# Optimization experiments

Hardware: AMD Instinct MI355X
Metric: run time of the kernel (lower is better)

The kernel has to match this reference:

```python
import jax, jax.numpy as jnp
import numpy as np

B, DIM, HEADS, H, W = 8, 384, 8, 128, 128
EPS = 1e-12  # torch F.normalize eps


def _conv1x1(x, w):
    # x: [b,c,h,w], w: [out,in] -> [b,out,h,w]
    return jnp.einsum('oc,bchw->bohw', w, x)


def _dwconv3x3(x, w):
    # depthwise 3x3, groups=DIM; w: [DIM,1,3,3]
    return jax.lax.conv_general_dilated(
        x, w, window_strides=(1, 1), padding='SAME',
        feature_group_count=DIM,
        dimension_numbers=('NCHW', 'OIHW', 'NCHW'))


def _l2norm(t):
    # F.normalize along last dim
    n = jnp.sqrt(jnp.sum(t * t, axis=-1, keepdims=True))
    return t / jnp.maximum(n, EPS)


def setup_inputs() -> dict:
    key = jax.random.key(0)
    ks = jax.random.split(key, 9)
    s = 0.02
    return {
        'x': jax.random.normal(ks[0], (B, DIM, H, W), jnp.float32),
        'w0': jax.random.normal(ks[1], (DIM, DIM), jnp.float32) * s,
        'w1': jax.random.normal(ks[2], (DIM, DIM), jnp.float32) * s,
        'w2': jax.random.normal(ks[3], (DIM, DIM), jnp.float32) * s,
        'dw0': jax.random.normal(ks[4], (DIM, 1, 3, 3), jnp.float32) * s,
        'dw1': jax.random.normal(ks[5], (DIM, 1, 3, 3), jnp.float32) * s,
        'dw2': jax.random.normal(ks[6], (DIM, 1, 3, 3), jnp.float32) * s,
        'wproj': jax.random.normal(ks[7], (DIM, DIM), jnp.float32) * s,
        'temp': jnp.ones((HEADS, 1, 1), jnp.float32),
    }


def reference(x, w0, w1, w2, dw0, dw1, dw2, wproj, temp):
    b, c, h, w = x.shape
    ch = c // HEADS
    q = _dwconv3x3(_conv1x1(x, w0), dw0)
    k = _dwconv3x3(_conv1x1(x, w1), dw1)
    v = _dwconv3x3(_conv1x1(x, w2), dw2)
    # b (head c) h w -> b head c (h w)
    q = _l2norm(q.reshape(b, HEADS, ch, h * w))
    k = _l2norm(k.reshape(b, HEADS, ch, h * w))
    v = v.reshape(b, HEADS, ch, h * w)
    attn = jax.nn.softmax(jnp.einsum('bhcn,bhdn->bhcd', q, k) * temp, axis=-1)
    out = jnp.einsum('bhcd,bhdn->bhcn', attn, v).reshape(b, c, h, w)
    return _conv1x1(out, wproj)
```

## Files before the change

kernel.cpp:

```cpp
#include <hip/hip_runtime.h>
#include <math.h>

#define DIMC 384
#define NHEADS 8
#define CHD 48
#define HWN 16384
#define IMW 128
#define PERT ((size_t)DIMC * HWN)
#define WELEM (DIMC * DIMC)
#define NB 8

typedef short short8 __attribute__((ext_vector_type(8)));
typedef unsigned short u16x8 __attribute__((ext_vector_type(8)));
typedef float f32x4 __attribute__((ext_vector_type(4)));

__device__ __forceinline__ unsigned short f2bf(float f) {
  unsigned int u = __float_as_uint(f);
  unsigned int r = (u + 0x7fffu + ((u >> 16) & 1u)) >> 16;
  return (unsigned short)r;
}
__device__ __forceinline__ float bf2f(unsigned short b) {
  return __uint_as_float(((unsigned int)b) << 16);
}
__device__ __forceinline__ void async16(const void* g, void* l) {
  __builtin_amdgcn_global_load_lds(
      (const __attribute__((address_space(1))) void*)g,
      (__attribute__((address_space(3))) void*)l, 16, 0, 0);
}

template <int OUTBF>
__device__ __forceinline__ void mfma_gemm(
    const unsigned short* __restrict__ A,
    const unsigned short* __restrict__ BT,
    void* __restrict__ Y, int obase, int nbase)
{
  __shared__ unsigned short As[3][8192];
  __shared__ unsigned short Bs[3][16384];
  const int tid = threadIdx.x;
  const int lane = tid & 63;
  const int wv = tid >> 6;
  const int wm = (wv >> 2) * 64;
  const int wn = (wv & 3) * 64;

  f32x4 acc[4][4];
#pragma unroll
  for (int i = 0; i < 4; ++i)
#pragma unroll
    for (int j = 0; j < 4; ++j) acc[i][j] = (f32x4){0.f, 0.f, 0.f, 0.f};

  const int srow = tid >> 3;
  const int sks = (tid & 7) * 8;
  const unsigned short* asrc = A + (size_t)(obase + srow) * DIMC + sks;
  const unsigned short* bsrc = BT + (size_t)(nbase + srow) * DIMC + sks;

  const int ar = wm + (lane & 15);
  const int br = wn + (lane & 15);
  const int kg = (lane >> 4) << 4;
  const int sw = (lane & 7) << 4;

#define WAITVM(n) asm volatile("s_waitcnt vmcnt(" #n ")" ::: "memory")
#define SBAR()                                 \
  do {                                         \
    __builtin_amdgcn_sched_barrier(0);         \
    __builtin_amdgcn_s_barrier();              \
    __builtin_amdgcn_sched_barrier(0);         \
  } while (0)

#define STAGE(buf, k0)                                                   \
  do {                                                                   \
    _Pragma("unroll") for (int i = 0; i < 2; ++i)                        \
        async16(asrc + (size_t)(i * 64) * DIMC + (k0),                   \
                &As[buf][(size_t)(tid + i * 512) * 8]);                  \
    _Pragma("unroll") for (int i = 0; i < 4; ++i)                        \
        async16(bsrc + (size_t)(i * 64) * DIMC + (k0),                   \
                &Bs[buf][(size_t)(tid + i * 512) * 8]);                  \
  } while (0)

#define COMPUTE(buf)                                                     \
  do {                                                                   \
    short8 af[2][4], bf[2][4];                                           \
    _Pragma("unroll") for (int kq = 0; kq < 2; ++kq) {                   \
      const int kb = kq * 64 + kg;                                       \
      _Pragma("unroll") for (int mi = 0; mi < 4; ++mi)                   \
          af[kq][mi] = *reinterpret_cast<const short8*>(                 \
              (const char*)&As[buf][0] + (ar + mi * 16) * 128 + (kb ^ sw)); \
      _Pragma("unroll") for (int ni = 0; ni < 4; ++ni)                   \
          bf[kq][ni] = *reinterpret_cast<const short8*>(                 \
              (const char*)&Bs[buf][0] + (br + ni * 16) * 128 + (kb ^ sw)); \
    }                                                                    \
    __builtin_amdgcn_s_setprio(1);                                       \
    _Pragma("unroll") for (int kq = 0; kq < 2; ++kq)                     \
      _Pragma("unroll") for (int mi = 0; mi < 4; ++mi)                   \
        _Pragma("unroll") for (int ni = 0; ni < 4; ++ni)                 \
          acc[mi][ni] = __builtin_amdgcn_mfma_f32_16x16x32_bf16(         \
              af[kq][mi], bf[kq][ni], acc[mi][ni], 0, 0, 0);             \
    __builtin_amdgcn_s_setprio(0);                                       \
  } while (0)

  STAGE(0, 0);
  STAGE(1, 64);

  WAITVM(6); SBAR(); STAGE(2, 128); COMPUTE(0);
  WAITVM(6); SBAR(); STAGE(0, 192); COMPUTE(1);
  WAITVM(6); SBAR(); STAGE(1, 256); COMPUTE(2);
  WAITVM(6); SBAR(); STAGE(2, 320); COMPUTE(0);
  WAITVM(6); SBAR(); COMPUTE(1);
  WAITVM(0); SBAR(); COMPUTE(2);

#undef STAGE
#undef COMPUTE
#undef WAITVM
#undef SBAR

  const int orow = obase + wm + ((lane >> 4) << 2);
  const int ocol = nbase + wn + (lane & 15);
#pragma unroll
  for (int mi = 0; mi < 4; ++mi)
#pragma unroll
    for (int ni = 0; ni < 4; ++ni)
#pragma unroll
      for (int r = 0; r < 4; ++r) {
        size_t off = (size_t)(orow + mi * 16 + r) * HWN + ocol + ni * 16;
        if (OUTBF) ((unsigned short*)Y)[off] = f2bf(acc[mi][ni][r]);
        else       ((float*)Y)[off] = acc[mi][ni][r];
      }
}

__global__ __launch_bounds__(512) void k_conv_mfma(
    const unsigned short* __restrict__ Wc, const unsigned short* __restrict__ XT,
    unsigned short* __restrict__ Y)
{
  int lin = ((int)blockIdx.z * 64 + blockIdx.y) * 9 + blockIdx.x;
  int swz = (lin & 7) * 576 + (lin >> 3);
  int g = swz / 9, r = swz - g * 9;
  int bb = g >> 6, nt = g & 63;
  int j = r / 3, mt = r - j * 3;
  mfma_gemm<1>(Wc + j * WELEM, XT + (size_t)bb * PERT,
               Y + (size_t)bb * 3 * PERT + (size_t)j * PERT, mt * 128, nt * 256);
}

__global__ __launch_bounds__(512) void k_final_mfma(
    const unsigned short* __restrict__ M, const unsigned short* __restrict__ vT,
    float* __restrict__ out)
{
  int lin = ((int)blockIdx.z * 64 + blockIdx.y) * 3 + blockIdx.x;
  int swz = (lin & 7) * 192 + (lin >> 3);
  int g = swz / 3, mt = swz - g * 3;
  int bb = g >> 6, nt = g & 63;
  mfma_gemm<0>(M + (size_t)bb * WELEM, vT + (size_t)bb * PERT,
               out + (size_t)bb * PERT, mt * 128, nt * 256);
}

__global__ __launch_bounds__(256) void k_transpose_x(
    const float* __restrict__ x, unsigned short* __restrict__ XT)
{
  __shared__ unsigned short S[64][72];
  int n0 = blockIdx.x * 64, c0 = blockIdx.y * 64;
  const float* xb = x + (size_t)blockIdx.z * PERT;
  unsigned short* XTb = XT + (size_t)blockIdx.z * PERT;
  int t = threadIdx.x;
  int cl = t >> 2, ns = (t & 3) * 16;
  const float* src = &xb[(size_t)(c0 + cl) * HWN + n0 + ns];
#pragma unroll
  for (int i = 0; i < 16; i += 4) {
    float4 v = *reinterpret_cast<const float4*>(&src[i]);
    S[cl][ns + i + 0] = f2bf(v.x);
    S[cl][ns + i + 1] = f2bf(v.y);
    S[cl][ns + i + 2] = f2bf(v.z);
    S[cl][ns + i + 3] = f2bf(v.w);
  }
  __syncthreads();
  int nl = t >> 2, cs = (t & 3) * 16;
  unsigned short tmp[16];
#pragma unroll
  for (int i = 0; i < 16; ++i) tmp[i] = S[cs + i][nl];
  u16x8 p0, p1;
#pragma unroll
  for (int i = 0; i < 8; ++i) { p0[i] = tmp[i]; p1[i] = tmp[8 + i]; }
  char* rowb = (char*)XTb + (size_t)(n0 + nl) * (DIMC * 2);
  int cb = (c0 + cs) * 2;
  int sw = (nl & 7) << 4;
  *reinterpret_cast<u16x8*>(rowb + ((cb) ^ sw)) = p0;
  *reinterpret_cast<u16x8*>(rowb + ((cb + 16) ^ sw)) = p1;
}

__global__ __launch_bounds__(256) void k_transpose_v(
    const unsigned short* __restrict__ qkv, unsigned short* __restrict__ vT)
{
  __shared__ unsigned short S[64][72];
  int n0 = blockIdx.x * 64, c0 = blockIdx.y * 64;
  const unsigned short* v = qkv + (size_t)blockIdx.z * 3 * PERT + 2 * PERT;
  unsigned short* vTb = vT + (size_t)blockIdx.z * PERT;
  int t = threadIdx.x;
  int cl = t >> 2, ns = (t & 3) * 16;
  const unsigned short* src = &v[(size_t)(c0 + cl) * HWN + n0 + ns];
  *reinterpret_cast<u16x8*>(&S[cl][ns]) = *reinterpret_cast<const u16x8*>(&src[0]);
  *reinterpret_cast<u16x8*>(&S[cl][ns + 8]) = *reinterpret_cast<const u16x8*>(&src[8]);
  __syncthreads();
  int nl = t >> 2, cs = (t & 3) * 16;
  unsigned short tmp[16];
#pragma unroll
  for (int i = 0; i < 16; ++i) tmp[i] = S[cs + i][nl];
  u16x8 p0, p1;
#pragma unroll
  for (int i = 0; i < 8; ++i) { p0[i] = tmp[i]; p1[i] = tmp[8 + i]; }
  char* rowb = (char*)vTb + (size_t)(n0 + nl) * (DIMC * 2);
  int cb = (c0 + cs) * 2;
  int sw = (nl & 7) << 4;
  *reinterpret_cast<u16x8*>(rowb + ((cb) ^ sw)) = p0;
  *reinterpret_cast<u16x8*>(rowb + ((cb + 16) ^ sw)) = p1;
}

__global__ __launch_bounds__(256) void k_convert_w(
    const float* __restrict__ w0, const float* __restrict__ w1,
    const float* __restrict__ w2, unsigned short* __restrict__ Wc)
{
  int idx = blockIdx.x * 256 + threadIdx.x;
  int j = idx / WELEM, r = idx - j * WELEM;
  int m = r / DIMC, k = r - m * DIMC;
  const float* s = (j == 0) ? w0 : (j == 1) ? w1 : w2;
  int kd = (k & ~63) | ((k & 63) ^ ((m & 7) << 3));
  Wc[j * WELEM + m * DIMC + kd] = f2bf(s[r]);
}

__global__ __launch_bounds__(256) void k_dwconv(
    const unsigned short* __restrict__ Yin, const float* __restrict__ dw0,
    const float* __restrict__ dw1, const float* __restrict__ dw2,
    unsigned short* __restrict__ Zout, float* __restrict__ partial)
{
  __shared__ float red[4];
  int gid = blockIdx.x * 256 + threadIdx.x;
  int plane = gid >> 10;
  int rem = gid & 1023;
  int pl = plane % (3 * DIMC);
  int j = pl / DIMC;
  int c = pl - j * DIMC;
  int h = rem >> 3;
  int wg = (rem & 7) << 4;
  int lane = threadIdx.x & 63;
  const float* dw = ((j == 0) ? dw0 : (j == 1) ? dw1 : dw2) + c * 9;
  const unsigned short* src = Yin + (size_t)plane * HWN;

  float acc[16];
#pragma unroll
  for (int i = 0; i < 16; ++i) acc[i] = 0.f;

#pragma unroll
  for (int dy = -1; dy <= 1; ++dy) {
    int hh = h + dy;
    bool valid = (hh >= 0) && (hh < IMW);
    float mf[16];
    if (valid) {
      const unsigned short* row = src + hh * IMW + wg;
      u16x8 a0 = *reinterpret_cast<const u16x8*>(row);
      u16x8 a1 = *reinterpret_cast<const u16x8*>(row + 8);
#pragma unroll
      for (int i = 0; i < 8; ++i) { mf[i] = bf2f(a0[i]); mf[8 + i] = bf2f(a1[i]); }
    } else {
#pragma unroll
      for (int i = 0; i < 16; ++i) mf[i] = 0.f;
    }
    float lf = __shfl_up(mf[15], 1);
    float rf = __shfl_down(mf[0], 1);
    if ((lane & 7) == 0) lf = 0.f;
    if ((lane & 7) == 7) rf = 0.f;
    float t0 = dw[(dy + 1) * 3], t1 = dw[(dy + 1) * 3 + 1], t2 = dw[(dy + 1) * 3 + 2];
    acc[0] = fmaf(lf, t0, fmaf(mf[0], t1, fmaf(mf[1], t2, acc[0])));
#pragma unroll
    for (int i = 1; i < 15; ++i)
      acc[i] = fmaf(mf[i - 1], t0, fmaf(mf[i], t1, fmaf(mf[i + 1], t2, acc[i])));
    acc[15] = fmaf(mf[14], t0, fmaf(mf[15], t1, fmaf(rf, t2, acc[15])));
  }

  u16x8 o0, o1;
#pragma unroll
  for (int i = 0; i < 8; ++i) { o0[i] = f2bf(acc[i]); o1[i] = f2bf(acc[8 + i]); }
  unsigned short* dst = Zout + (size_t)plane * HWN + h * IMW + wg;
  *reinterpret_cast<u16x8*>(dst) = o0;
  *reinterpret_cast<u16x8*>(dst + 8) = o1;

  if (j < 2) {
    float s = 0.f;
#pragma unroll
    for (int i = 0; i < 16; ++i) s = fmaf(acc[i], acc[i], s);
#pragma unroll
    for (int off = 32; off > 0; off >>= 1) s += __shfl_down(s, off);
    if ((threadIdx.x & 63) == 0) red[threadIdx.x >> 6] = s;
    __syncthreads();
    if (threadIdx.x == 0)
      partial[blockIdx.x] = red[0] + red[1] + red[2] + red[3];
  }
}

__global__ __launch_bounds__(256) void k_qk_mfma(
    const unsigned short* __restrict__ qkv, float* __restrict__ Spart)
{
  __shared__ float Sred[4][2304];
  int blk = blockIdx.x;
  int b = blk >> 6, h = (blk >> 3) & 7, slice = blk & 7;
  int tid = threadIdx.x, lane = tid & 63, w = tid >> 6;
  const unsigned short* qb = qkv + ((size_t)b * 3 * DIMC + h * CHD) * HWN;
  const unsigned short* kb = qb + (size_t)DIMC * HWN;
  const int row = lane & 15;
  const int ko = (lane >> 4) << 3;
  const int n0 = slice * 2048 + w * 512;

  f32x4 acc[3][3];
#pragma unroll
  for (int i = 0; i < 3; ++i)
#pragma unroll
    for (int j = 0; j < 3; ++j) acc[i][j] = (f32x4){0.f, 0.f, 0.f, 0.f};

  for (int ns = n0; ns < n0 + 512; ns += 32) {
    short8 aq[3], bk[3];
#pragma unroll
    for (int mi = 0; mi < 3; ++mi)
      aq[mi] = *reinterpret_cast<const short8*>(&qb[(size_t)(mi * 16 + row) * HWN + ns + ko]);
#pragma unroll
    for (int ni = 0; ni < 3; ++ni)
      bk[ni] = *reinterpret_cast<const short8*>(&kb[(size_t)(ni * 16 + row) * HWN + ns + ko]);
#pragma unroll
    for (int mi = 0; mi < 3; ++mi)
#pragma unroll
      for (int ni = 0; ni < 3; ++ni)
        acc[mi][ni] = __builtin_amdgcn_mfma_f32_16x16x32_bf16(
            aq[mi], bk[ni], acc[mi][ni], 0, 0, 0);
  }
  const int c0 = (lane >> 4) << 2;
#pragma unroll
  for (int mi = 0; mi < 3; ++mi)
#pragma unroll
    for (int ni = 0; ni < 3; ++ni)
#pragma unroll
      for (int r = 0; r < 4; ++r)
        Sred[w][(mi * 16 + c0 + r) * 48 + ni * 16 + row] = acc[mi][ni][r];
  __syncthreads();
  float* dst = Spart + (size_t)blk * 2304;
#pragma unroll
  for (int i = 0; i < 9; ++i) {
    int e = tid + i * 256;
    dst[e] = Sred[0][e] + Sred[1][e] + Sred[2][e] + Sred[3][e];
  }
}

__global__ __launch_bounds__(384) void k_attn_sm(
    const float* __restrict__ Spart, const float* __restrict__ partial,
    const float* __restrict__ temp, float* __restrict__ Aat)
{
  __shared__ float sk[DIMC];
  int b = blockIdx.x, t = threadIdx.x;
  int h = t / CHD, c = t - h * CHD;
  float sq = 0.f, skk = 0.f;
#pragma unroll
  for (int s = 0; s < 4; ++s) {
    sq  += partial[((size_t)b * 1152 + t) * 4 + s];
    skk += partial[((size_t)b * 1152 + DIMC + t) * 4 + s];
  }
  sk[t] = 1.f / fmaxf(sqrtf(skk), 1e-12f);
  float invq = 1.f / fmaxf(sqrtf(sq), 1e-12f);
  __syncthreads();
  float vals[CHD];
#pragma unroll
  for (int d = 0; d < CHD; ++d) vals[d] = 0.f;
  for (int sl = 0; sl < 8; ++sl) {
    const float* sp = Spart + (size_t)(b * 64 + h * 8 + sl) * 2304 + c * 48;
#pragma unroll
    for (int d = 0; d < CHD; ++d) vals[d] += sp[d];
  }
  float tp = temp[h];
  float vq = invq * tp;
  float mx = -1e30f;
#pragma unroll
  for (int d = 0; d < CHD; ++d) {
    vals[d] *= vq * sk[h * CHD + d];
    mx = fmaxf(mx, vals[d]);
  }
  float sum = 0.f;
#pragma unroll
  for (int d = 0; d < CHD; ++d) { vals[d] = expf(vals[d] - mx); sum += vals[d]; }
  float inv = 1.f / sum;
  float* Arow = Aat + ((size_t)(b * 8 + h) * 48 + c) * 48;
#pragma unroll
  for (int d = 0; d < CHD; ++d) Arow[d] = vals[d] * inv;
}

__global__ __launch_bounds__(256) void k_combine(
    const float* __restrict__ wproj, const float* __restrict__ Aat,
    unsigned short* __restrict__ M)
{
  int idx = blockIdx.x * 256 + threadIdx.x;
  int b = idx / WELEM;
  int r2 = idx - b * WELEM;
  int o = r2 / DIMC;
  int dg = r2 - o * DIMC;
  int h = dg / CHD, d = dg - h * CHD;
  const float* wrow = wproj + (size_t)o * DIMC + h * CHD;
  const float* Acol = Aat + (size_t)b * DIMC * CHD + (size_t)(h * CHD) * CHD + d;
  float s = 0.f;
#pragma unroll
  for (int c = 0; c < CHD; ++c)
    s = fmaf(wrow[c], Acol[c * CHD], s);
  int dd = (dg & ~63) | ((dg & 63) ^ ((o & 7) << 3));
  M[b * WELEM + o * DIMC + dd] = f2bf(s);
}

extern "C" void kernel_launch(void* const* d_in, const int* in_sizes, int n_in,
                              void* d_out, int out_size, void* d_ws, size_t ws_size,
                              hipStream_t stream)
{
  const float* x     = (const float*)d_in[0];
  const float* w0    = (const float*)d_in[1];
  const float* w1    = (const float*)d_in[2];
  const float* w2    = (const float*)d_in[3];
  const float* dw0   = (const float*)d_in[4];
  const float* dw1   = (const float*)d_in[5];
  const float* dw2   = (const float*)d_in[6];
  const float* wproj = (const float*)d_in[7];
  const float* temp  = (const float*)d_in[8];
  float* out = (float*)d_out;

  char* p = (char*)d_ws;
  unsigned short* Wc     = (unsigned short*)p;  p += (size_t)3 * WELEM * 2;
  unsigned short* XT     = (unsigned short*)p;  p += (size_t)NB * PERT * 2;
  unsigned short* q0k0v0 = (unsigned short*)p;  p += (size_t)NB * 3 * PERT * 2;
  unsigned short* qkv    = (unsigned short*)p;  p += (size_t)NB * 3 * PERT * 2;
  float* Spart   = (float*)p;  p += (size_t)512 * 2304 * 4;
  float* Aat     = (float*)p;  p += (size_t)NB * DIMC * CHD * 4;
  float* partial = (float*)p;  p += (size_t)NB * 3 * DIMC * 4 * 4;
  unsigned short* Mbf = (unsigned short*)p;
  unsigned short* vT = XT;

  k_convert_w<<<(3 * WELEM + 255) / 256, 256, 0, stream>>>(w0, w1, w2, Wc);
  k_transpose_x<<<dim3(256, 6, NB), 256, 0, stream>>>(x, XT);
  k_conv_mfma<<<dim3(9, 64, NB), 512, 0, stream>>>(Wc, XT, q0k0v0);
  k_dwconv<<<NB * 3 * DIMC * 4, 256, 0, stream>>>(q0k0v0, dw0, dw1, dw2, qkv, partial);
  k_transpose_v<<<dim3(256, 6, NB), 256, 0, stream>>>(qkv, vT);
  k_qk_mfma<<<512, 256, 0, stream>>>(qkv, Spart);
  k_attn_sm<<<NB, 384, 0, stream>>>(Spart, partial, temp, Aat);
  k_combine<<<(NB * WELEM) / 256, 256, 0, stream>>>(wproj, Aat, Mbf);
  k_final_mfma<<<dim3(3, 64, NB), 512, 0, stream>>>(Mbf, vT, out);
  (void)in_sizes; (void)n_in; (void)out_size; (void)ws_size;
}
```

Baseline: 650.6 us.

## Shrink GEMM tiles to 128x128 with double buffering and LDS-staged coalesced epilogue

Both MFMA GEMM kernels drop from 512-thread 128x256 tiles with triple-buffered LDS to 256-thread 128x128 tiles with double buffering in a 64KB LDS region, doubling the grid. The epilogue now stages accumulators through padded LDS and writes whole rows with 16-byte vector stores, replacing scattered per-element global stores. The smaller tile and fewer LDS bytes per block are meant to raise occupancy and coalesce output writes. In exchange the pipeline waits for vmcnt(0) every step, so loads overlap compute less, and each B element is reloaded more often.

Result: slower. 724.8 us (+11.4%).

```diff
diff --git a/kernel.cpp b/kernel.cpp
--- a/kernel.cpp
+++ b/kernel.cpp
@@ -34,13 +34,12 @@
     const unsigned short* __restrict__ BT,
     void* __restrict__ Y, int obase, int nbase)
 {
-  __shared__ unsigned short As[3][8192];
-  __shared__ unsigned short Bs[3][16384];
+  __shared__ unsigned char LDSRAW[65536];
   const int tid = threadIdx.x;
   const int lane = tid & 63;
   const int wv = tid >> 6;
-  const int wm = (wv >> 2) * 64;
-  const int wn = (wv & 3) * 64;
+  const int wm = (wv >> 1) * 64;
+  const int wn = (wv & 1) * 64;
 
   f32x4 acc[4][4];
 #pragma unroll
@@ -66,89 +65,122 @@
     __builtin_amdgcn_sched_barrier(0);         \
   } while (0)
 
-#define STAGE(buf, k0)                                                   \
-  do {                                                                   \
-    _Pragma("unroll") for (int i = 0; i < 2; ++i)                        \
-        async16(asrc + (size_t)(i * 64) * DIMC + (k0),                   \
-                &As[buf][(size_t)(tid + i * 512) * 8]);                  \
-    _Pragma("unroll") for (int i = 0; i < 4; ++i)                        \
-        async16(bsrc + (size_t)(i * 64) * DIMC + (k0),                   \
-                &Bs[buf][(size_t)(tid + i * 512) * 8]);                  \
+#define STAGE(buf, k0)                                                    \
+  do {                                                                    \
+    unsigned short* Adst = (unsigned short*)LDSRAW + (buf) * 8192;        \
+    unsigned short* Bdst = (unsigned short*)(LDSRAW + 32768) + (buf) * 8192; \
+    _Pragma("unroll") for (int i = 0; i < 4; ++i)                         \
+        async16(asrc + (size_t)(i * 32) * DIMC + (k0),                    \
+                Adst + (size_t)(tid + i * 256) * 8);                      \
+    _Pragma("unroll") for (int i = 0; i < 4; ++i)                         \
+        async16(bsrc + (size_t)(i * 32) * DIMC + (k0),                    \
+                Bdst + (size_t)(tid + i * 256) * 8);                      \
   } while (0)
 
-#define COMPUTE(buf)                                                     \
-  do {                                                                   \
-    short8 af[2][4], bf[2][4];                                           \
-    _Pragma("unroll") for (int kq = 0; kq < 2; ++kq) {                   \
-      const int kb = kq * 64 + kg;                                       \
-      _Pragma("unroll") for (int mi = 0; mi < 4; ++mi)                   \
-          af[kq][mi] = *reinterpret_cast<const short8*>(                 \
-              (const char*)&As[buf][0] + (ar + mi * 16) * 128 + (kb ^ sw)); \
-      _Pragma("unroll") for (int ni = 0; ni < 4; ++ni)                   \
-          bf[kq][ni] = *reinterpret_cast<const short8*>(                 \
-              (const char*)&Bs[buf][0] + (br + ni * 16) * 128 + (kb ^ sw)); \
-    }                                                                    \
-    __builtin_amdgcn_s_setprio(1);                                       \
-    _Pragma("unroll") for (int kq = 0; kq < 2; ++kq)                     \
-      _Pragma("unroll") for (int mi = 0; mi < 4; ++mi)                   \
-        _Pragma("unroll") for (int ni = 0; ni < 4; ++ni)                 \
-          acc[mi][ni] = __builtin_amdgcn_mfma_f32_16x16x32_bf16(         \
-              af[kq][mi], bf[kq][ni], acc[mi][ni], 0, 0, 0);             \
-    __builtin_amdgcn_s_setprio(0);                                       \
+#define COMPUTE(buf)                                                      \
+  do {                                                                    \
+    const char* Ab = (const char*)LDSRAW + (buf) * 16384;                 \
+    const char* Bb = (const char*)LDSRAW + 32768 + (buf) * 16384;         \
+    short8 af[2][4], bf[2][4];                                            \
+    _Pragma("unroll") for (int kq = 0; kq < 2; ++kq) {                    \
+      const int kb = kq * 64 + kg;                                        \
+      _Pragma("unroll") for (int mi = 0; mi < 4; ++mi)                    \
+          af[kq][mi] = *reinterpret_cast<const short8*>(                  \
+              Ab + (ar + mi * 16) * 128 + (kb ^ sw));                     \
+      _Pragma("unroll") for (int ni = 0; ni < 4; ++ni)                    \
+          bf[kq][ni] = *reinterpret_cast<const short8*>(                  \
+              Bb + (br + ni * 16) * 128 + (kb ^ sw));                     \
+    }                                                                     \
+    __builtin_amdgcn_s_setprio(1);                                        \
+    _Pragma("unroll") for (int kq = 0; kq < 2; ++kq)                      \
+      _Pragma("unroll") for (int mi = 0; mi < 4; ++mi)                    \
+        _Pragma("unroll") for (int ni = 0; ni < 4; ++ni)                  \
+          acc[mi][ni] = __builtin_amdgcn_mfma_f32_16x16x32_bf16(          \
+              af[kq][mi], bf[kq][ni], acc[mi][ni], 0, 0, 0);              \
+    __builtin_amdgcn_s_setprio(0);                                        \
   } while (0)
 
   STAGE(0, 0);
-  STAGE(1, 64);
-
-  WAITVM(6); SBAR(); STAGE(2, 128); COMPUTE(0);
-  WAITVM(6); SBAR(); STAGE(0, 192); COMPUTE(1);
-  WAITVM(6); SBAR(); STAGE(1, 256); COMPUTE(2);
-  WAITVM(6); SBAR(); STAGE(2, 320); COMPUTE(0);
-  WAITVM(6); SBAR(); COMPUTE(1);
-  WAITVM(0); SBAR(); COMPUTE(2);
+  WAITVM(0); SBAR(); STAGE(1, 64);  COMPUTE(0);
+  WAITVM(0); SBAR(); STAGE(0, 128); COMPUTE(1);
+  WAITVM(0); SBAR(); STAGE(1, 192); COMPUTE(0);
+  WAITVM(0); SBAR(); STAGE(0, 256); COMPUTE(1);
+  WAITVM(0); SBAR(); STAGE(1, 320); COMPUTE(0);
+  WAITVM(0); SBAR();                COMPUTE(1);
+  __syncthreads();
 
 #undef STAGE
 #undef COMPUTE
+
+  const int crow = wm + ((lane >> 4) << 2);
+  const int ccol = wn + (lane & 15);
+
+  if (OUTBF) {
+    unsigned short* C16 = (unsigned short*)LDSRAW;
+#pragma unroll
+    for (int mi = 0; mi < 4; ++mi)
+#pragma unroll
+      for (int ni = 0; ni < 4; ++ni)
+#pragma unroll
+        for (int r = 0; r < 4; ++r)
+          C16[(crow + mi * 16 + r) * 134 + ccol + ni * 16] = f2bf(acc[mi][ni][r]);
+    __syncthreads();
+    const int row = tid >> 1, col = (tid & 1) << 6;
+    const unsigned short* srcl = C16 + row * 134 + col;
+    unsigned short* dst = (unsigned short*)Y + (size_t)(obase + row) * HWN + nbase + col;
+#pragma unroll
+    for (int i = 0; i < 8; ++i)
+      *reinterpret_cast<u16x8*>(dst + i * 8) = *reinterpret_cast<const u16x8*>(srcl + i * 8);
+  } else {
+    float* C32 = (float*)LDSRAW;
+#pragma unroll
+    for (int p = 0; p < 2; ++p) {
+      if (wn == p * 64) {
+#pragma unroll
+        for (int mi = 0; mi < 4; ++mi)
+#pragma unroll
+          for (int ni = 0; ni < 4; ++ni)
+#pragma unroll
+            for (int r = 0; r < 4; ++r)
+              C32[(crow + mi * 16 + r) * 66 + (lane & 15) + ni * 16] = acc[mi][ni][r];
+      }
+      __syncthreads();
+      const int row = tid >> 1, colseg = (tid & 1) << 5;
+      const float* srcl = C32 + row * 66 + colseg;
+      float* dst = (float*)Y + (size_t)(obase + row) * HWN + nbase + p * 64 + colseg;
+#pragma unroll
+      for (int i = 0; i < 8; ++i)
+        *reinterpret_cast<f32x4*>(dst + i * 4) = *reinterpret_cast<const f32x4*>(srcl + i * 4);
+      __syncthreads();
+    }
+  }
 #undef WAITVM
 #undef SBAR
-
-  const int orow = obase + wm + ((lane >> 4) << 2);
-  const int ocol = nbase + wn + (lane & 15);
-#pragma unroll
-  for (int mi = 0; mi < 4; ++mi)
-#pragma unroll
-    for (int ni = 0; ni < 4; ++ni)
-#pragma unroll
-      for (int r = 0; r < 4; ++r) {
-        size_t off = (size_t)(orow + mi * 16 + r) * HWN + ocol + ni * 16;
-        if (OUTBF) ((unsigned short*)Y)[off] = f2bf(acc[mi][ni][r]);
-        else       ((float*)Y)[off] = acc[mi][ni][r];
-      }
-}
-
-__global__ __launch_bounds__(512) void k_conv_mfma(
+}
+
+__global__ __launch_bounds__(256) void k_conv_mfma(
     const unsigned short* __restrict__ Wc, const unsigned short* __restrict__ XT,
     unsigned short* __restrict__ Y)
 {
-  int lin = ((int)blockIdx.z * 64 + blockIdx.y) * 9 + blockIdx.x;
-  int swz = (lin & 7) * 576 + (lin >> 3);
+  int lin = ((int)blockIdx.z * 128 + blockIdx.y) * 9 + blockIdx.x;
+  int swz = (lin & 7) * 1152 + (lin >> 3);
   int g = swz / 9, r = swz - g * 9;
-  int bb = g >> 6, nt = g & 63;
+  int bb = g >> 7, nt = g & 127;
   int j = r / 3, mt = r - j * 3;
   mfma_gemm<1>(Wc + j * WELEM, XT + (size_t)bb * PERT,
-               Y + (size_t)bb * 3 * PERT + (size_t)j * PERT, mt * 128, nt * 256);
-}
-
-__global__ __launch_bounds__(512) void k_final_mfma(
+               Y + (size_t)bb * 3 * PERT + (size_t)j * PERT, mt * 128, nt * 128);
+}
+
+__global__ __launch_bounds__(256) void k_final_mfma(
     const unsigned short* __restrict__ M, const unsigned short* __restrict__ vT,
     float* __restrict__ out)
 {
-  int lin = ((int)blockIdx.z * 64 + blockIdx.y) * 3 + blockIdx.x;
-  int swz = (lin & 7) * 192 + (lin >> 3);
+  int lin = ((int)blockIdx.z * 128 + blockIdx.y) * 3 + blockIdx.x;
+  int swz = (lin & 7) * 384 + (lin >> 3);
   int g = swz / 3, mt = swz - g * 3;
-  int bb = g >> 6, nt = g & 63;
+  int bb = g >> 7, nt = g & 127;
   mfma_gemm<0>(M + (size_t)bb * WELEM, vT + (size_t)bb * PERT,
-               out + (size_t)bb * PERT, mt * 128, nt * 256);
+               out + (size_t)bb * PERT, mt * 128, nt * 128);
 }
 
 __global__ __launch_bounds__(256) void k_transpose_x(
@@ -432,12 +464,12 @@
 
   k_convert_w<<<(3 * WELEM + 255) / 256, 256, 0, stream>>>(w0, w1, w2, Wc);
   k_transpose_x<<<dim3(256, 6, NB), 256, 0, stream>>>(x, XT);
-  k_conv_mfma<<<dim3(9, 64, NB), 512, 0, stream>>>(Wc, XT, q0k0v0);
+  k_conv_mfma<<<dim3(9, 128, NB), 256, 0, stream>>>(Wc, XT, q0k0v0);
   k_dwconv<<<NB * 3 * DIMC * 4, 256, 0, stream>>>(q0k0v0, dw0, dw1, dw2, qkv, partial);
   k_transpose_v<<<dim3(256, 6, NB), 256, 0, stream>>>(qkv, vT);
   k_qk_mfma<<<512, 256, 0, stream>>>(qkv, Spart);
   k_attn_sm<<<NB, 384, 0, stream>>>(Spart, partial, temp, Aat);
   k_combine<<<(NB * WELEM) / 256, 256, 0, stream>>>(wproj, Aat, Mbf);
-  k_final_mfma<<<dim3(3, 64, NB), 512, 0, stream>>>(Mbf, vT, out);
+  k_final_mfma<<<dim3(3, 128, NB), 256, 0, stream>>>(Mbf, vT, out);
   (void)in_sizes; (void)n_in; (void)out_size; (void)ws_size;
 }
```

## Load GEMM A-operand weights directly into registers, bypassing LDS staging

Applied to the files above, without the earlier changes.

The MFMA GEMM no longer stages the weight (A) tiles through LDS. Each wave loads its A fragments straight from global memory into two double-buffered register sets, interleaved with the existing triple-buffered LDS pipeline for B. The pre-swizzle of weights in k_convert_w and k_combine is removed because the A path no longer reads from swizzled LDS, and the vmcnt waits are retuned for the extra loads. This cuts LDS traffic and footprint for A, relying on the small weight matrices being served from cache. In exchange it raises register pressure and issues more, less coalesced global loads per wave.

New measurement: 760.8 us. 1.17x slower.

```diff
diff --git a/kernel.cpp b/kernel.cpp
--- a/kernel.cpp
+++ b/kernel.cpp
@@ -34,7 +34,6 @@
     const unsigned short* __restrict__ BT,
     void* __restrict__ Y, int obase, int nbase)
 {
-  __shared__ unsigned short As[3][8192];
   __shared__ unsigned short Bs[3][16384];
   const int tid = threadIdx.x;
   const int lane = tid & 63;
@@ -50,13 +49,16 @@
 
   const int srow = tid >> 3;
   const int sks = (tid & 7) * 8;
-  const unsigned short* asrc = A + (size_t)(obase + srow) * DIMC + sks;
   const unsigned short* bsrc = BT + (size_t)(nbase + srow) * DIMC + sks;
 
-  const int ar = wm + (lane & 15);
+  const unsigned short* aP =
+      A + (size_t)(obase + wm + (lane & 15)) * DIMC + ((lane >> 4) << 3);
+
   const int br = wn + (lane & 15);
   const int kg = (lane >> 4) << 4;
   const int sw = (lane & 7) << 4;
+
+  short8 sA0[2][4], sA1[2][4];
 
 #define WAITVM(n) asm volatile("s_waitcnt vmcnt(" #n ")" ::: "memory")
 #define SBAR()                                 \
@@ -66,24 +68,26 @@
     __builtin_amdgcn_sched_barrier(0);         \
   } while (0)
 
-#define STAGE(buf, k0)                                                   \
+#define STAGE_B(buf, k0)                                                 \
   do {                                                                   \
-    _Pragma("unroll") for (int i = 0; i < 2; ++i)                        \
-        async16(asrc + (size_t)(i * 64) * DIMC + (k0),                   \
-                &As[buf][(size_t)(tid + i * 512) * 8]);                  \
     _Pragma("unroll") for (int i = 0; i < 4; ++i)                        \
         async16(bsrc + (size_t)(i * 64) * DIMC + (k0),                   \
                 &Bs[buf][(size_t)(tid + i * 512) * 8]);                  \
   } while (0)
 
-#define COMPUTE(buf)                                                     \
+#define LOADA(set, k0)                                                   \
   do {                                                                   \
-    short8 af[2][4], bf[2][4];                                           \
+    _Pragma("unroll") for (int kq = 0; kq < 2; ++kq)                     \
+      _Pragma("unroll") for (int mi = 0; mi < 4; ++mi)                   \
+        set[kq][mi] = *reinterpret_cast<const short8*>(                  \
+            aP + (size_t)(mi * 16) * DIMC + (k0) + kq * 32);             \
+  } while (0)
+
+#define COMPUTE(buf, set)                                                \
+  do {                                                                   \
+    short8 bf[2][4];                                                     \
     _Pragma("unroll") for (int kq = 0; kq < 2; ++kq) {                   \
       const int kb = kq * 64 + kg;                                       \
-      _Pragma("unroll") for (int mi = 0; mi < 4; ++mi)                   \
-          af[kq][mi] = *reinterpret_cast<const short8*>(                 \
-              (const char*)&As[buf][0] + (ar + mi * 16) * 128 + (kb ^ sw)); \
       _Pragma("unroll") for (int ni = 0; ni < 4; ++ni)                   \
           bf[kq][ni] = *reinterpret_cast<const short8*>(                 \
               (const char*)&Bs[buf][0] + (br + ni * 16) * 128 + (kb ^ sw)); \
@@ -93,21 +97,22 @@
       _Pragma("unroll") for (int mi = 0; mi < 4; ++mi)                   \
         _Pragma("unroll") for (int ni = 0; ni < 4; ++ni)                 \
           acc[mi][ni] = __builtin_amdgcn_mfma_f32_16x16x32_bf16(         \
-              af[kq][mi], bf[kq][ni], acc[mi][ni], 0, 0, 0);             \
+              set[kq][mi], bf[kq][ni], acc[mi][ni], 0, 0, 0);            \
     __builtin_amdgcn_s_setprio(0);                                       \
   } while (0)
 
-  STAGE(0, 0);
-  STAGE(1, 64);
-
-  WAITVM(6); SBAR(); STAGE(2, 128); COMPUTE(0);
-  WAITVM(6); SBAR(); STAGE(0, 192); COMPUTE(1);
-  WAITVM(6); SBAR(); STAGE(1, 256); COMPUTE(2);
-  WAITVM(6); SBAR(); STAGE(2, 320); COMPUTE(0);
-  WAITVM(6); SBAR(); COMPUTE(1);
-  WAITVM(0); SBAR(); COMPUTE(2);
-
-#undef STAGE
+  STAGE_B(0, 0);   LOADA(sA0, 0);
+  STAGE_B(1, 64);  LOADA(sA1, 64);
+
+  WAITVM(12); SBAR(); STAGE_B(2, 128); COMPUTE(0, sA0); LOADA(sA0, 128);
+  WAITVM(20); SBAR(); STAGE_B(0, 192); COMPUTE(1, sA1); LOADA(sA1, 192);
+  WAITVM(20); SBAR(); STAGE_B(1, 256); COMPUTE(2, sA0); LOADA(sA0, 256);
+  WAITVM(20); SBAR(); STAGE_B(2, 320); COMPUTE(0, sA1); LOADA(sA1, 320);
+  WAITVM(20); SBAR();                  COMPUTE(1, sA0);
+  WAITVM(8);  SBAR();                  COMPUTE(2, sA1);
+
+#undef STAGE_B
+#undef LOADA
 #undef COMPUTE
 #undef WAITVM
 #undef SBAR
@@ -217,10 +222,8 @@
 {
   int idx = blockIdx.x * 256 + threadIdx.x;
   int j = idx / WELEM, r = idx - j * WELEM;
-  int m = r / DIMC, k = r - m * DIMC;
   const float* s = (j == 0) ? w0 : (j == 1) ? w1 : w2;
-  int kd = (k & ~63) | ((k & 63) ^ ((m & 7) << 3));
-  Wc[j * WELEM + m * DIMC + kd] = f2bf(s[r]);
+  Wc[idx] = f2bf(s[r]);
 }
 
 __global__ __launch_bounds__(256) void k_dwconv(
@@ -400,8 +403,7 @@
 #pragma unroll
   for (int c = 0; c < CHD; ++c)
     s = fmaf(wrow[c], Acol[c * CHD], s);
-  int dd = (dg & ~63) | ((dg & 63) ^ ((o & 7) << 3));
-  M[b * WELEM + o * DIMC + dd] = f2bf(s);
+  M[idx] = f2bf(s);
 }
 
 extern "C" void kernel_launch(void* const* d_in, const int* in_sizes, int n_in,
```

## Retile 1x1-conv GEMMs to full 384-row M tiles with double-buffered K pipeline

Applied to the files above, without the earlier changes.

The shared MFMA GEMM moves from 128x256 tiles with triple buffering to tiles covering all 384 output channels by 128 pixels, with double buffering. Each block now reads each activation column once instead of three times (once per M tile), which cuts global and L2 traffic for the activation operand. Each wave holds a 96x64 accumulator (24 MFMA tiles), and the grids and swizzles are remapped to match. The cost is more registers per wave and only two pipeline stages, which can lower occupancy and leave load latency less hidden.

Result: faster. 580.4 us (-10.8%).

```diff
diff --git a/kernel.cpp b/kernel.cpp
--- a/kernel.cpp
+++ b/kernel.cpp
@@ -29,29 +29,28 @@
 }
 
 template <int OUTBF>
-__device__ __forceinline__ void mfma_gemm(
+__device__ __forceinline__ void gemm384_body(
     const unsigned short* __restrict__ A,
     const unsigned short* __restrict__ BT,
-    void* __restrict__ Y, int obase, int nbase)
-{
-  __shared__ unsigned short As[3][8192];
-  __shared__ unsigned short Bs[3][16384];
+    void* __restrict__ Y, int nbase)
+{
+  __shared__ unsigned short As[2][24576];
+  __shared__ unsigned short Bs[2][8192];
   const int tid = threadIdx.x;
   const int lane = tid & 63;
   const int wv = tid >> 6;
-  const int wm = (wv >> 2) * 64;
-  const int wn = (wv & 3) * 64;
-
-  f32x4 acc[4][4];
-#pragma unroll
-  for (int i = 0; i < 4; ++i)
+  const int wm = (wv >> 1) * 96;
+  const int wn = (wv & 1) * 64;
+
+  f32x4 acc[6][4];
+#pragma unroll
+  for (int i = 0; i < 6; ++i)
 #pragma unroll
     for (int j = 0; j < 4; ++j) acc[i][j] = (f32x4){0.f, 0.f, 0.f, 0.f};
 
-  const int srow = tid >> 3;
-  const int sks = (tid & 7) * 8;
-  const unsigned short* asrc = A + (size_t)(obase + srow) * DIMC + sks;
-  const unsigned short* bsrc = BT + (size_t)(nbase + srow) * DIMC + sks;
+  const unsigned short* asrc = A + (size_t)(tid >> 3) * DIMC + (tid & 7) * 8;
+  const unsigned short* bsrc =
+      BT + (size_t)(nbase + (tid >> 3)) * DIMC + (tid & 7) * 8;
 
   const int ar = wm + (lane & 15);
   const int br = wn + (lane & 15);
@@ -68,20 +67,20 @@
 
 #define STAGE(buf, k0)                                                   \
   do {                                                                   \
-    _Pragma("unroll") for (int i = 0; i < 2; ++i)                        \
+    _Pragma("unroll") for (int i = 0; i < 6; ++i)                        \
         async16(asrc + (size_t)(i * 64) * DIMC + (k0),                   \
                 &As[buf][(size_t)(tid + i * 512) * 8]);                  \
-    _Pragma("unroll") for (int i = 0; i < 4; ++i)                        \
+    _Pragma("unroll") for (int i = 0; i < 2; ++i)                        \
         async16(bsrc + (size_t)(i * 64) * DIMC + (k0),                   \
                 &Bs[buf][(size_t)(tid + i * 512) * 8]);                  \
   } while (0)
 
 #define COMPUTE(buf)                                                     \
   do {                                                                   \
-    short8 af[2][4], bf[2][4];                                           \
+    short8 af[2][6], bf[2][4];                                           \
     _Pragma("unroll") for (int kq = 0; kq < 2; ++kq) {                   \
       const int kb = kq * 64 + kg;                                       \
-      _Pragma("unroll") for (int mi = 0; mi < 4; ++mi)                   \
+      _Pragma("unroll") for (int mi = 0; mi < 6; ++mi)                   \
           af[kq][mi] = *reinterpret_cast<const short8*>(                 \
               (const char*)&As[buf][0] + (ar + mi * 16) * 128 + (kb ^ sw)); \
       _Pragma("unroll") for (int ni = 0; ni < 4; ++ni)                   \
@@ -90,7 +89,7 @@
     }                                                                    \
     __builtin_amdgcn_s_setprio(1);                                       \
     _Pragma("unroll") for (int kq = 0; kq < 2; ++kq)                     \
-      _Pragma("unroll") for (int mi = 0; mi < 4; ++mi)                   \
+      _Pragma("unroll") for (int mi = 0; mi < 6; ++mi)                   \
         _Pragma("unroll") for (int ni = 0; ni < 4; ++ni)                 \
           acc[mi][ni] = __builtin_amdgcn_mfma_f32_16x16x32_bf16(         \
               af[kq][mi], bf[kq][ni], acc[mi][ni], 0, 0, 0);             \
@@ -98,24 +97,23 @@
   } while (0)
 
   STAGE(0, 0);
-  STAGE(1, 64);
-
-  WAITVM(6); SBAR(); STAGE(2, 128); COMPUTE(0);
-  WAITVM(6); SBAR(); STAGE(0, 192); COMPUTE(1);
-  WAITVM(6); SBAR(); STAGE(1, 256); COMPUTE(2);
-  WAITVM(6); SBAR(); STAGE(2, 320); COMPUTE(0);
-  WAITVM(6); SBAR(); COMPUTE(1);
-  WAITVM(0); SBAR(); COMPUTE(2);
+  WAITVM(0); SBAR();
+  STAGE(1, 64);            COMPUTE(0);
+  SBAR(); STAGE(0, 128); WAITVM(8); SBAR(); COMPUTE(1);
+  SBAR(); STAGE(1, 192); WAITVM(8); SBAR(); COMPUTE(0);
+  SBAR(); STAGE(0, 256); WAITVM(8); SBAR(); COMPUTE(1);
+  SBAR(); STAGE(1, 320); WAITVM(8); SBAR(); COMPUTE(0);
+  WAITVM(0); SBAR(); COMPUTE(1);
 
 #undef STAGE
 #undef COMPUTE
 #undef WAITVM
 #undef SBAR
 
-  const int orow = obase + wm + ((lane >> 4) << 2);
+  const int orow = wm + ((lane >> 4) << 2);
   const int ocol = nbase + wn + (lane & 15);
 #pragma unroll
-  for (int mi = 0; mi < 4; ++mi)
+  for (int mi = 0; mi < 6; ++mi)
 #pragma unroll
     for (int ni = 0; ni < 4; ++ni)
 #pragma unroll
@@ -130,25 +128,24 @@
     const unsigned short* __restrict__ Wc, const unsigned short* __restrict__ XT,
     unsigned short* __restrict__ Y)
 {
-  int lin = ((int)blockIdx.z * 64 + blockIdx.y) * 9 + blockIdx.x;
-  int swz = (lin & 7) * 576 + (lin >> 3);
-  int g = swz / 9, r = swz - g * 9;
-  int bb = g >> 6, nt = g & 63;
-  int j = r / 3, mt = r - j * 3;
-  mfma_gemm<1>(Wc + j * WELEM, XT + (size_t)bb * PERT,
-               Y + (size_t)bb * 3 * PERT + (size_t)j * PERT, mt * 128, nt * 256);
+  int g0 = (int)blockIdx.y * 128 + blockIdx.x;
+  int lin = g0 * 3 + blockIdx.z;
+  int swz = (lin & 7) * 384 + (lin >> 3);
+  int g = swz / 3, j = swz - g * 3;
+  int bb = g >> 7, nt = g & 127;
+  gemm384_body<1>(Wc + j * WELEM, XT + (size_t)bb * PERT,
+                  Y + (size_t)bb * 3 * PERT + (size_t)j * PERT, nt * 128);
 }
 
 __global__ __launch_bounds__(512) void k_final_mfma(
     const unsigned short* __restrict__ M, const unsigned short* __restrict__ vT,
     float* __restrict__ out)
 {
-  int lin = ((int)blockIdx.z * 64 + blockIdx.y) * 3 + blockIdx.x;
-  int swz = (lin & 7) * 192 + (lin >> 3);
-  int g = swz / 3, mt = swz - g * 3;
-  int bb = g >> 6, nt = g & 63;
-  mfma_gemm<0>(M + (size_t)bb * WELEM, vT + (size_t)bb * PERT,
-               out + (size_t)bb * PERT, mt * 128, nt * 256);
+  int lin = (int)blockIdx.y * 128 + blockIdx.x;
+  int swz = (lin & 7) * 128 + (lin >> 3);
+  int bb = swz >> 7, nt = swz & 127;
+  gemm384_body<0>(M + (size_t)bb * WELEM, vT + (size_t)bb * PERT,
+                  out + (size_t)bb * PERT, nt * 128);
 }
 
 __global__ __launch_bounds__(256) void k_transpose_x(
@@ -432,12 +429,12 @@
 
   k_convert_w<<<(3 * WELEM + 255) / 256, 256, 0, stream>>>(w0, w1, w2, Wc);
   k_transpose_x<<<dim3(256, 6, NB), 256, 0, stream>>>(x, XT);
-  k_conv_mfma<<<dim3(9, 64, NB), 512, 0, stream>>>(Wc, XT, q0k0v0);
+  k_conv_mfma<<<dim3(128, NB, 3), 512, 0, stream>>>(Wc, XT, q0k0v0);
   k_dwconv<<<NB * 3 * DIMC * 4, 256, 0, stream>>>(q0k0v0, dw0, dw1, dw2, qkv, partial);
   k_transpose_v<<<dim3(256, 6, NB), 256, 0, stream>>>(qkv, vT);
   k_qk_mfma<<<512, 256, 0, stream>>>(qkv, Spart);
   k_attn_sm<<<NB, 384, 0, stream>>>(Spart, partial, temp, Aat);
   k_combine<<<(NB * WELEM) / 256, 256, 0, stream>>>(wproj, Aat, Mbf);
-  k_final_mfma<<<dim3(3, 64, NB), 512, 0, stream>>>(Mbf, vT, out);
+  k_final_mfma<<<dim3(128, NB), 512, 0, stream>>>(Mbf, vT, out);
   (void)in_sizes; (void)n_in; (void)out_size; (void)ws_size;
 }
```
